# Optimization experiments

Measured on AMD Instinct MI355X. Metric: run time of the kernel, lower is better.

Reference implementation:

```python
import jax, jax.numpy as jnp
import numpy as np
from functools import partial

# Block hyperparams (match init_kwargs)
B, C, N, H = 16, 512, 1024, 8
HID = 4 * C
TAU, THRESH, SG_SCALE = 2.0, 1.0, 5.0
ATTN_SCALE = 0.25
BN_EPS = 1e-5

# LIF spiking neuron (single-step, stateless): membrane v = x / tau, hard threshold
# forward; sigmoid surrogate gradient (scale=5.0) in backward.
@partial(jax.custom_vjp, nondiff_argnums=(1,))
def spike(u, scale):
    return (u >= 0.0).astype(u.dtype)

def _spike_fwd(u, scale):
    return spike(u, scale), u

def _spike_bwd(scale, u, g):
    s = jax.nn.sigmoid(scale * u)
    return (g * scale * s * (1.0 - s),)

spike.defvjp(_spike_fwd, _spike_bwd)

def lif(x):
    return spike(x / TAU - THRESH, SG_SCALE)

def conv1x1(x, w, b=None):
    # x: [B,C,N], w: [O,C] -> [B,O,N]
    y = jnp.einsum('oc,bcn->bon', w, x)
    return y if b is None else y + b[None, :, None]

def bn(x, g, b):
    # BatchNorm1d, training-mode batch stats over (batch, length), biased var
    m = jnp.mean(x, axis=(0, 2), keepdims=True)
    v = jnp.var(x, axis=(0, 2), keepdims=True)
    return (x - m) * jax.lax.rsqrt(v + BN_EPS) * g[None, :, None] + b[None, :, None]


def setup_inputs() -> dict:
    key = jax.random.key(0)
    ks = jax.random.split(key, 8)
    w = lambda k, o, i: jax.random.normal(k, (o, i), dtype=jnp.float32) * 0.02
    inp = {
        'x': jax.random.normal(ks[0], (B, C, N), dtype=jnp.float32),
        'q_w': w(ks[1], C, C), 'q_g': jnp.ones((C,), jnp.float32), 'q_b': jnp.zeros((C,), jnp.float32),
        'k_w': w(ks[2], C, C), 'k_g': jnp.ones((C,), jnp.float32), 'k_b': jnp.zeros((C,), jnp.float32),
        'v_w': w(ks[3], C, C), 'v_g': jnp.ones((C,), jnp.float32), 'v_b': jnp.zeros((C,), jnp.float32),
        'proj_w': w(ks[4], C, C), 'proj_bias': jnp.zeros((C,), jnp.float32),
        'proj_g': jnp.ones((C,), jnp.float32), 'proj_b': jnp.zeros((C,), jnp.float32),
        'fc1_w': w(ks[5], HID, C), 'fc1_bias': jnp.zeros((HID,), jnp.float32),
        'fc1_g': jnp.ones((HID,), jnp.float32), 'fc1_b': jnp.zeros((HID,), jnp.float32),
        'fc2_w': w(ks[6], C, HID), 'fc2_bias': jnp.zeros((C,), jnp.float32),
        'fc2_g': jnp.ones((C,), jnp.float32), 'fc2_b': jnp.zeros((C,), jnp.float32),
    }
    return inp


def reference(x, q_w, q_g, q_b, k_w, k_g, k_b, v_w, v_g, v_b,
              proj_w, proj_bias, proj_g, proj_b,
              fc1_w, fc1_bias, fc1_g, fc1_b, fc2_w, fc2_bias, fc2_g, fc2_b):
    Bb, Cc, Nn = x.shape
    D = Cc // H

    def heads(t):  # [B,C,N] -> [B,H,N,D]
        return t.transpose(0, 2, 1).reshape(Bb, Nn, H, D).transpose(0, 2, 1, 3)

    # spiking attention (no softmax): (Q K^T) V * 0.25
    q = heads(lif(bn(conv1x1(x, q_w), q_g, q_b)))
    k = heads(lif(bn(conv1x1(x, k_w), k_g, k_b)))
    v = heads(lif(bn(conv1x1(x, v_w), v_g, v_b)))
    scores = jnp.einsum('bhnd,bhmd->bhnm', q, k)            # [B,H,N,N]
    attn = jnp.einsum('bhnm,bhmd->bhnd', scores, v) * ATTN_SCALE
    a = attn.transpose(0, 1, 3, 2).reshape(Bb, Cc, Nn)       # [B,C,N]
    a = lif(a)
    a = lif(bn(conv1x1(a, proj_w, proj_bias), proj_g, proj_b))
    x = x + a                                                # residual 1

    # conv1x1-BN-LIF MLP
    h = lif(bn(conv1x1(x, fc1_w, fc1_bias), fc1_g, fc1_b))
    h = lif(bn(conv1x1(h, fc2_w, fc2_bias), fc2_g, fc2_b))
    return x + h                                             # residual 2
```

## Files before the change

kernel.cpp:

```cpp
#include <hip/hip_runtime.h>
#include <stdint.h>

#pragma clang fp contract(off)

#define BATCH 16
#define CCH   512
#define NLEN  1024
#define NH    8
#define DH    64

__device__ float pw128(const float* __restrict__ x) {
    float r0=x[0],r1=x[1],r2=x[2],r3=x[3],r4=x[4],r5=x[5],r6=x[6],r7=x[7];
    for (int i = 8; i < 128; i += 8) {
        r0 += x[i+0]; r1 += x[i+1]; r2 += x[i+2]; r3 += x[i+3];
        r4 += x[i+4]; r5 += x[i+5]; r6 += x[i+6]; r7 += x[i+7];
    }
    return ((r0+r1)+(r2+r3))+((r4+r5)+(r6+r7));
}
__device__ float pw128_sqdev(const float* __restrict__ x, float m) {
    float r0,r1,r2,r3,r4,r5,r6,r7;
    {
        float d;
        d = x[0]-m; r0 = d*d;  d = x[1]-m; r1 = d*d;
        d = x[2]-m; r2 = d*d;  d = x[3]-m; r3 = d*d;
        d = x[4]-m; r4 = d*d;  d = x[5]-m; r5 = d*d;
        d = x[6]-m; r6 = d*d;  d = x[7]-m; r7 = d*d;
    }
    for (int i = 8; i < 128; i += 8) {
        float d;
        d = x[i+0]-m; r0 += d*d;  d = x[i+1]-m; r1 += d*d;
        d = x[i+2]-m; r2 += d*d;  d = x[i+3]-m; r3 += d*d;
        d = x[i+4]-m; r4 += d*d;  d = x[i+5]-m; r5 += d*d;
        d = x[i+6]-m; r6 += d*d;  d = x[i+7]-m; r7 += d*d;
    }
    return ((r0+r1)+(r2+r3))+((r4+r5)+(r6+r7));
}

__global__ __launch_bounds__(64) void bn_stats_np_k(const float* __restrict__ Y, int O,
                                                    float2* __restrict__ st)
{
    const int o = blockIdx.x;
    const int t = threadIdx.x;
    const int bi = t >> 2, q = t & 3;
    __shared__ float part[64];
    __shared__ float msh;
    const float* p = Y + ((size_t)bi * O + o) * NLEN + q * 256;
    {
        float s0 = pw128(p), s1 = pw128(p + 128);
        part[t] = s0 + s1;
    }
    __syncthreads();
    if (t == 0) {
        float s = 0.0f;
        for (int b = 0; b < 16; ++b) {
            const float* pp = &part[b * 4];
            float v = (pp[0] + pp[1]) + (pp[2] + pp[3]);
            s = (b == 0) ? v : (s + v);
        }
        msh = s / 16384.0f;
    }
    __syncthreads();
    const float m = msh;
    {
        float s0 = pw128_sqdev(p, m), s1 = pw128_sqdev(p + 128, m);
        part[t] = s0 + s1;
    }
    __syncthreads();
    if (t == 0) {
        float s = 0.0f;
        for (int b = 0; b < 16; ++b) {
            const float* pp = &part[b * 4];
            float v = (pp[0] + pp[1]) + (pp[2] + pp[3]);
            s = (b == 0) ? v : (s + v);
        }
        float var = s / 16384.0f;
        float ve  = var + 1e-5f;
        float sq  = (float)sqrt((double)ve);
        float r   = (float)(1.0 / (double)sq);
        st[o] = make_float2(m, r);
    }
}

__device__ inline bool spike_f32(float y, float2 s, float g, float b) {
    float t1 = y - s.x;
    float t2 = t1 * s.y;
    float t3 = t2 * g;
    float t4 = t3 + b;
    float u  = t4 / 2.0f - 1.0f;
    return u >= 0.0f;
}

template<int MODE>
__global__ __launch_bounds__(256) void gemm_k(
    const float* __restrict__ W, const float* __restrict__ Xf, const uint8_t* __restrict__ Xs8,
    const float* __restrict__ bias, float* __restrict__ Y,
    int O, int Cin, int N)
{
    __shared__ float Ws[32][132];
    __shared__ float Xs[32][132];
    const int b = blockIdx.z;
    const size_t xbase = (size_t)b * Cin * N;
    float* Yb = Y + (size_t)b * O * N;
    const int o0 = blockIdx.y * 128;
    const int n0 = blockIdx.x * 128;
    const int t  = threadIdx.x;
    const int tx = t & 15;
    const int ty = t >> 4;

    const int wr = t >> 1;
    const int wk = (t & 1) << 4;
    const int xk = t >> 3;
    const int xc = (t & 7) << 4;

    float acc[8][8];
#pragma unroll
    for (int i = 0; i < 8; ++i)
#pragma unroll
        for (int j = 0; j < 8; ++j) acc[i][j] = 0.0f;

    float4 wA[4];
    float  xr[16];

    auto loadG = [&](int k0) {
        const float* wp = W + (size_t)(o0 + wr) * Cin + k0 + wk;
#pragma unroll
        for (int j = 0; j < 4; ++j)
            wA[j] = *reinterpret_cast<const float4*>(wp + 4 * j);
        size_t off = xbase + (size_t)(k0 + xk) * N + n0 + xc;
#pragma unroll
        for (int j = 0; j < 4; ++j) {
            float4 v = *reinterpret_cast<const float4*>(Xf + off + 4 * j);
            if (MODE == 0) {
                xr[4*j+0]=v.x; xr[4*j+1]=v.y; xr[4*j+2]=v.z; xr[4*j+3]=v.w;
            } else {
                uchar4 u = *reinterpret_cast<const uchar4*>(Xs8 + off + 4 * j);
                xr[4*j+0]=v.x+(float)u.x; xr[4*j+1]=v.y+(float)u.y;
                xr[4*j+2]=v.z+(float)u.z; xr[4*j+3]=v.w+(float)u.w;
            }
        }
    };
    auto stage = [&]() {
#pragma unroll
        for (int j = 0; j < 4; ++j) {
            Ws[wk+4*j+0][wr] = wA[j].x;
            Ws[wk+4*j+1][wr] = wA[j].y;
            Ws[wk+4*j+2][wr] = wA[j].z;
            Ws[wk+4*j+3][wr] = wA[j].w;
        }
#pragma unroll
        for (int j = 0; j < 4; ++j)
            *reinterpret_cast<float4*>(&Xs[xk][xc + 4*j]) =
                make_float4(xr[4*j+0], xr[4*j+1], xr[4*j+2], xr[4*j+3]);
    };

    loadG(0);
    stage();
    __syncthreads();
    for (int k0 = 0;;) {
        const int kn = k0 + 32;
        const bool more = kn < Cin;
        if (more) loadG(kn);
#pragma unroll
        for (int kk = 0; kk < 32; ++kk) {
            float4 a0 = *reinterpret_cast<const float4*>(&Ws[kk][ty * 4]);
            float4 a1 = *reinterpret_cast<const float4*>(&Ws[kk][64 + ty * 4]);
            float4 b0 = *reinterpret_cast<const float4*>(&Xs[kk][tx * 4]);
            float4 b1 = *reinterpret_cast<const float4*>(&Xs[kk][64 + tx * 4]);
            float av[8] = {a0.x,a0.y,a0.z,a0.w,a1.x,a1.y,a1.z,a1.w};
            float bv[8] = {b0.x,b0.y,b0.z,b0.w,b1.x,b1.y,b1.z,b1.w};
#pragma unroll
            for (int i = 0; i < 8; ++i)
#pragma unroll
                for (int j = 0; j < 8; ++j)
                    acc[i][j] = fmaf(av[i], bv[j], acc[i][j]);
        }
        if (!more) break;
        __syncthreads();
        stage();
        __syncthreads();
        k0 = kn;
    }
#pragma unroll
    for (int half = 0; half < 2; ++half)
#pragma unroll
        for (int i = 0; i < 4; ++i) {
            const int r = half * 4 + i;
            const int o = o0 + half * 64 + ty * 4 + i;
            const float bb = bias ? bias[o] : 0.0f;
            float* yp = Yb + (size_t)o * N + n0;
            float4 r0, r1;
            r0.x = acc[r][0] + bb; r0.y = acc[r][1] + bb;
            r0.z = acc[r][2] + bb; r0.w = acc[r][3] + bb;
            r1.x = acc[r][4] + bb; r1.y = acc[r][5] + bb;
            r1.z = acc[r][6] + bb; r1.w = acc[r][7] + bb;
            *reinterpret_cast<float4*>(yp + tx * 4)      = r0;
            *reinterpret_cast<float4*>(yp + 64 + tx * 4) = r1;
        }
}

__global__ __launch_bounds__(256) void wt_k(const float* __restrict__ W, float* __restrict__ Wt,
                                            int O, int Cin)
{
    __shared__ float tile[32][33];
    const int k0 = blockIdx.x * 32, o0 = blockIdx.y * 32;
    const int tx = threadIdx.x & 31, ty = threadIdx.x >> 5;
#pragma unroll
    for (int j = 0; j < 4; ++j)
        tile[ty + 8*j][tx] = W[(size_t)(o0 + ty + 8*j) * Cin + k0 + tx];
    __syncthreads();
#pragma unroll
    for (int j = 0; j < 4; ++j)
        Wt[(size_t)(k0 + ty + 8*j) * O + o0 + tx] = tile[tx][ty + 8*j];
}

__global__ __launch_bounds__(256) void col_bits_k(const uint8_t* __restrict__ S,
                                                  unsigned long long* __restrict__ bits, int Cin)
{
    const int n0 = blockIdx.x * 64, kw = blockIdx.y, b = blockIdx.z;
    __shared__ uint8_t tile[64][64];
    const int t = threadIdx.x;
    const int r = t >> 2, cg = (t & 3) * 16;
    const uint8_t* src = S + ((size_t)b * Cin + kw * 64 + r) * NLEN + n0 + cg;
    *reinterpret_cast<uint4*>(&tile[r][cg]) = *reinterpret_cast<const uint4*>(src);
    __syncthreads();
    if (t < 64) {
        unsigned long long m = 0;
#pragma unroll
        for (int rr = 0; rr < 64; ++rr)
            m |= ((unsigned long long)(tile[rr][t] != 0)) << rr;
        bits[((size_t)b * NLEN + n0 + t) * (Cin >> 6) + kw] = m;
    }
}

__global__ __launch_bounds__(256) void sparse_gemm_k(
    const float* __restrict__ Wt, const unsigned long long* __restrict__ bits,
    const float* __restrict__ bias, float* __restrict__ Y, int Cin)
{
    const int wid  = (blockIdx.x << 2) + (threadIdx.x >> 6);
    const int lane = threadIdx.x & 63;
    const int b = wid >> 10, n = wid & 1023;
    const int W64 = Cin >> 6;
    float acc[8];
#pragma unroll
    for (int i = 0; i < 8; ++i) acc[i] = 0.0f;
    const unsigned long long* bp = bits + ((size_t)b * NLEN + n) * W64;
    for (int w = 0; w < W64; ++w) {
        unsigned long long m = bp[w];
        while (m) {
            const int bit = __builtin_ctzll(m);
            m &= m - 1;
            const int k = (w << 6) + bit;
            const float* wr = Wt + ((size_t)k << 9) + lane * 8;
            float4 w0 = *reinterpret_cast<const float4*>(wr);
            float4 w1 = *reinterpret_cast<const float4*>(wr + 4);
            acc[0] += w0.x; acc[1] += w0.y; acc[2] += w0.z; acc[3] += w0.w;
            acc[4] += w1.x; acc[5] += w1.y; acc[6] += w1.z; acc[7] += w1.w;
        }
    }
    const float* bq = bias + lane * 8;
    float4 b0 = *reinterpret_cast<const float4*>(bq);
    float4 b1 = *reinterpret_cast<const float4*>(bq + 4);
    float bi[8] = {b0.x, b0.y, b0.z, b0.w, b1.x, b1.y, b1.z, b1.w};
    float* yp = Y + ((size_t)b * 512 + lane * 8) * NLEN + n;
#pragma unroll
    for (int i = 0; i < 8; ++i)
        yp[(size_t)i * NLEN] = acc[i] + bi[i];
}

__global__ __launch_bounds__(256) void spike_pack_qkv_k(
    const float* __restrict__ Y, const float2* __restrict__ st,
    const float* __restrict__ gq, const float* __restrict__ gk, const float* __restrict__ gv,
    const float* __restrict__ bq, const float* __restrict__ bk, const float* __restrict__ bv,
    uint8_t* __restrict__ oq, uint8_t* __restrict__ ok, uint8_t* __restrict__ ov)
{
    const int nt = blockIdx.x, hs = blockIdx.y, b = blockIdx.z;
    const int tensor = hs >> 3, h = hs & 7;
    const float* g  = (tensor == 0) ? gq : (tensor == 1) ? gk : gv;
    const float* be = (tensor == 0) ? bq : (tensor == 1) ? bk : bv;
    uint8_t* outp   = (tensor == 0) ? oq : (tensor == 1) ? ok : ov;
    __shared__ uint8_t tile[64][68];
    const int t = threadIdx.x;
    {
        const int i = t & 63, dq = t >> 6;
#pragma unroll
        for (int p = 0; p < 16; ++p) {
            int d  = dq * 16 + p;
            int cf = hs * 64 + d;
            int cl = h * 64 + d;
            float y = Y[((size_t)b * 1536 + cf) * NLEN + nt * 64 + i];
            tile[d][i] = spike_f32(y, st[cf], g[cl], be[cl]) ? 1 : 0;
        }
    }
    __syncthreads();
    {
        const int d = t & 63, iq = t >> 6;
#pragma unroll
        for (int p = 0; p < 16; ++p) {
            int i = iq * 16 + p;
            outp[((size_t)(b * NH + h) * NLEN + nt * 64 + i) * DH + d] = tile[d][i];
        }
    }
}

__global__ __launch_bounds__(256) void ktv_k(const uint8_t* __restrict__ Kb, const uint8_t* __restrict__ Vb,
                                             float* __restrict__ M)
{
    const int bh = blockIdx.x;
    const uint8_t* kp = Kb + (size_t)bh * NLEN * DH;
    const uint8_t* vp = Vb + (size_t)bh * NLEN * DH;
    __shared__ float ks[64][68];
    __shared__ float vs[64][68];
    const int t = threadIdx.x;
    const int d2 = t & 63, g4 = t >> 6;
    float acc[16];
#pragma unroll
    for (int j = 0; j < 16; ++j) acc[j] = 0.f;

    for (int nc = 0; nc < NLEN; nc += 64) {
#pragma unroll
        for (int p = 0; p < 16; ++p) {
            int idx = t + p * 256;
            int r = idx >> 6, d = idx & 63;
            ks[r][d] = (float)kp[(size_t)(nc + r) * DH + d];
            vs[r][d] = (float)vp[(size_t)(nc + r) * DH + d];
        }
        __syncthreads();
        for (int n = 0; n < 64; ++n) {
            float vv = vs[n][d2];
#pragma unroll
            for (int j = 0; j < 16; ++j)
                acc[j] += ks[n][g4 * 16 + j] * vv;
        }
        __syncthreads();
    }
#pragma unroll
    for (int j = 0; j < 16; ++j)
        M[(size_t)bh * 4096 + (size_t)(g4 * 16 + j) * 64 + d2] = acc[j];
}

__global__ __launch_bounds__(256) void attn_spike_k(const uint8_t* __restrict__ Qb, const float* __restrict__ M,
                                                    uint8_t* __restrict__ A)
{
    const int nt = blockIdx.x, h = blockIdx.y, b = blockIdx.z;
    const int bh = b * NH + h;
    __shared__ float Ms[64][68];
    __shared__ float qs[64][65];
    const int t = threadIdx.x;
#pragma unroll
    for (int p = 0; p < 16; ++p) {
        int idx = t + p * 256;
        int r = idx >> 6, c = idx & 63;
        Ms[r][c] = M[(size_t)bh * 4096 + idx];
        qs[c][r] = (float)Qb[((size_t)bh * NLEN + nt * 64 + r) * DH + c];
    }
    __syncthreads();
    const int n = t & 63, dg = t >> 6;
    float acc[16];
#pragma unroll
    for (int j = 0; j < 16; ++j) acc[j] = 0.f;
    for (int d1 = 0; d1 < 64; ++d1) {
        float qv = qs[d1][n];
#pragma unroll
        for (int j = 0; j < 16; ++j)
            acc[j] += qv * Ms[d1][dg * 16 + j];
    }
#pragma unroll
    for (int j = 0; j < 16; ++j) {
        int d = dg * 16 + j;
        A[((size_t)b * CCH + h * 64 + d) * NLEN + nt * 64 + n] = (acc[j] >= 8.0f) ? 1 : 0;
    }
}

__global__ __launch_bounds__(256) void spike_store_k(
    const float* __restrict__ Y, const float2* __restrict__ st,
    const float* __restrict__ g, const float* __restrict__ bet,
    uint8_t* __restrict__ H, int Oc, int o_off, int Otot)
{
    size_t i4 = (size_t)blockIdx.x * 256 + threadIdx.x;
    size_t total = (size_t)BATCH * Oc * (NLEN / 4);
    if (i4 >= total) return;
    int n4 = (int)(i4 & 255);
    int o  = (int)((i4 >> 8) % Oc);
    int b  = (int)(i4 / ((size_t)256 * Oc));
    float4 y = reinterpret_cast<const float4*>(Y)[i4];
    float2 s = st[o];
    float gg = g[o], bb = bet[o];
    uchar4 r;
    r.x = spike_f32(y.x, s, gg, bb) ? 1 : 0;
    r.y = spike_f32(y.y, s, gg, bb) ? 1 : 0;
    r.z = spike_f32(y.z, s, gg, bb) ? 1 : 0;
    r.w = spike_f32(y.w, s, gg, bb) ? 1 : 0;
    *reinterpret_cast<uchar4*>(H + ((size_t)(b * Otot + o_off + o)) * NLEN + n4 * 4) = r;
}

__global__ __launch_bounds__(256) void final_k(
    const float* __restrict__ Y, const float2* __restrict__ st,
    const float* __restrict__ g, const float* __restrict__ bet,
    const float* __restrict__ x, const uint8_t* __restrict__ ares,
    float* __restrict__ Out)
{
    size_t i4 = (size_t)blockIdx.x * 256 + threadIdx.x;
    size_t total = (size_t)BATCH * CCH * (NLEN / 4);
    if (i4 >= total) return;
    int o = (int)((i4 >> 8) % CCH);
    float4 y  = reinterpret_cast<const float4*>(Y)[i4];
    float4 xv = reinterpret_cast<const float4*>(x)[i4];
    uchar4 av = reinterpret_cast<const uchar4*>(ares)[i4];
    float2 s = st[o];
    float gg = g[o], bb = bet[o];
    float4 r;
    {
        float x1;
        x1 = xv.x + (float)av.x; r.x = x1 + (spike_f32(y.x, s, gg, bb) ? 1.0f : 0.0f);
        x1 = xv.y + (float)av.y; r.y = x1 + (spike_f32(y.y, s, gg, bb) ? 1.0f : 0.0f);
        x1 = xv.z + (float)av.z; r.z = x1 + (spike_f32(y.z, s, gg, bb) ? 1.0f : 0.0f);
        x1 = xv.w + (float)av.w; r.w = x1 + (spike_f32(y.w, s, gg, bb) ? 1.0f : 0.0f);
    }
    reinterpret_cast<float4*>(Out)[i4] = r;
}

extern "C" void kernel_launch(void* const* d_in, const int* in_sizes, int n_in,
                              void* d_out, int out_size, void* d_ws, size_t ws_size,
                              hipStream_t stream)
{
    const float* x         = (const float*)d_in[0];
    const float* q_w       = (const float*)d_in[1];
    const float* q_g       = (const float*)d_in[2];
    const float* q_b       = (const float*)d_in[3];
    const float* k_w       = (const float*)d_in[4];
    const float* k_g       = (const float*)d_in[5];
    const float* k_b       = (const float*)d_in[6];
    const float* v_w       = (const float*)d_in[7];
    const float* v_g       = (const float*)d_in[8];
    const float* v_b       = (const float*)d_in[9];
    const float* proj_w    = (const float*)d_in[10];
    const float* proj_bias = (const float*)d_in[11];
    const float* proj_g    = (const float*)d_in[12];
    const float* proj_b    = (const float*)d_in[13];
    const float* fc1_w     = (const float*)d_in[14];
    const float* fc1_bias  = (const float*)d_in[15];
    const float* fc1_g     = (const float*)d_in[16];
    const float* fc1_b     = (const float*)d_in[17];
    const float* fc2_w     = (const float*)d_in[18];
    const float* fc2_bias  = (const float*)d_in[19];
    const float* fc2_g     = (const float*)d_in[20];
    const float* fc2_b     = (const float*)d_in[21];
    float* out = (float*)d_out;

    char* ws = (char*)d_ws;
    const size_t MiB = 1ull << 20;
    if (ws_size < 124 * MiB) return;

    float*    Yq    = (float*)(ws);
    float*    Af    = (float*)(ws);
    uint8_t*  ab    = (uint8_t*)(ws);
    uint8_t*  ares  = (uint8_t*)(ws + 64 * MiB);
    uint8_t*  hb    = (uint8_t*)(ws + 72 * MiB);
    uint8_t*  qb    = (uint8_t*)(ws + 96 * MiB);
    uint8_t*  kb    = (uint8_t*)(ws + 104 * MiB);
    uint8_t*  vb    = (uint8_t*)(ws + 112 * MiB);
    float*    Wt    = (float*)(ws + 104 * MiB);
    unsigned long long* bits = (unsigned long long*)(ws + 108 * MiB);
    float*    Wcat  = (float*)(ws + 120 * MiB);
    float*    Mbuf  = (float*)(ws + 120 * MiB);
    float2*   stats = (float2*)(ws + 123 * MiB);

    dim3 thr256(256);

    hipMemcpyAsync(Wcat,          q_w, (size_t)512 * 512 * 4, hipMemcpyDeviceToDevice, stream);
    hipMemcpyAsync(Wcat + 262144, k_w, (size_t)512 * 512 * 4, hipMemcpyDeviceToDevice, stream);
    hipMemcpyAsync(Wcat + 524288, v_w, (size_t)512 * 512 * 4, hipMemcpyDeviceToDevice, stream);
    gemm_k<0><<<dim3(8, 12, 16), thr256, 0, stream>>>(Wcat, x, nullptr, nullptr, Yq, 1536, 512, 1024);
    bn_stats_np_k<<<dim3(1536), dim3(64), 0, stream>>>(Yq, 1536, stats);
    spike_pack_qkv_k<<<dim3(16, 24, 16), thr256, 0, stream>>>(Yq, stats, q_g, k_g, v_g,
                                                              q_b, k_b, v_b, qb, kb, vb);

    ktv_k<<<dim3(128), thr256, 0, stream>>>(kb, vb, Mbuf);
    attn_spike_k<<<dim3(16, 8, 16), thr256, 0, stream>>>(qb, Mbuf, ab);

    wt_k<<<dim3(16, 16), thr256, 0, stream>>>(proj_w, Wt, 512, 512);
    col_bits_k<<<dim3(16, 8, 16), thr256, 0, stream>>>(ab, bits, 512);
    sparse_gemm_k<<<dim3(4096), thr256, 0, stream>>>(Wt, bits, proj_bias, Af, 512);
    bn_stats_np_k<<<dim3(512), dim3(64), 0, stream>>>(Af, 512, stats);
    spike_store_k<<<dim3(8192), thr256, 0, stream>>>(Af, stats, proj_g, proj_b, ares, 512, 0, 512);

    for (int ch = 0; ch < 2; ++ch) {
        gemm_k<2><<<dim3(8, 8, 16), thr256, 0, stream>>>(fc1_w + (size_t)ch * 1024 * 512, x, ares,
                                                         fc1_bias + ch * 1024, Af, 1024, 512, 1024);
        bn_stats_np_k<<<dim3(1024), dim3(64), 0, stream>>>(Af, 1024, stats);
        spike_store_k<<<dim3(16384), thr256, 0, stream>>>(Af, stats, fc1_g + ch * 1024, fc1_b + ch * 1024,
                                                          hb, 1024, ch * 1024, 2048);
    }

    wt_k<<<dim3(64, 16), thr256, 0, stream>>>(fc2_w, Wt, 512, 2048);
    col_bits_k<<<dim3(16, 32, 16), thr256, 0, stream>>>(hb, bits, 2048);
    sparse_gemm_k<<<dim3(4096), thr256, 0, stream>>>(Wt, bits, fc2_bias, Af, 2048);
    bn_stats_np_k<<<dim3(512), dim3(64), 0, stream>>>(Af, 512, stats);
    final_k<<<dim3(8192), thr256, 0, stream>>>(Af, stats, fc2_g, fc2_b, x, ares, out);
}
```

Measured before the change: 1.432 ms.

## Double-buffer GEMM shared tiles with K-step 16 and one barrier per step

Switches the fp32 GEMM kernel from a single 32-deep shared-memory tile to two 16-deep buffers. The next tile is staged into the alternate buffer right after compute, so each K step needs only one __syncthreads instead of two. Per-thread prefetch registers are halved. The trade-off is twice as many loop iterations and barriers over the same K range, with less unrolled work per step to hide global-load latency.

```diff
diff --git a/kernel.cpp b/kernel.cpp
--- a/kernel.cpp
+++ b/kernel.cpp
@@ -96,8 +96,8 @@
     const float* __restrict__ bias, float* __restrict__ Y,
     int O, int Cin, int N)
 {
-    __shared__ float Ws[32][132];
-    __shared__ float Xs[32][132];
+    __shared__ float Ws[2][16][132];
+    __shared__ float Xs[2][16][132];
     const int b = blockIdx.z;
     const size_t xbase = (size_t)b * Cin * N;
     float* Yb = Y + (size_t)b * O * N;
@@ -108,9 +108,9 @@
     const int ty = t >> 4;
 
     const int wr = t >> 1;
-    const int wk = (t & 1) << 4;
-    const int xk = t >> 3;
-    const int xc = (t & 7) << 4;
+    const int wk = (t & 1) << 3;
+    const int xk = t >> 4;
+    const int xc = (t & 15) << 3;
 
     float acc[8][8];
 #pragma unroll
@@ -118,54 +118,51 @@
 #pragma unroll
         for (int j = 0; j < 8; ++j) acc[i][j] = 0.0f;
 
-    float4 wA[4];
-    float  xr[16];
+    float4 wA[2];
+    float  xr[8];
 
     auto loadG = [&](int k0) {
         const float* wp = W + (size_t)(o0 + wr) * Cin + k0 + wk;
-#pragma unroll
-        for (int j = 0; j < 4; ++j)
-            wA[j] = *reinterpret_cast<const float4*>(wp + 4 * j);
+        wA[0] = *reinterpret_cast<const float4*>(wp);
+        wA[1] = *reinterpret_cast<const float4*>(wp + 4);
         size_t off = xbase + (size_t)(k0 + xk) * N + n0 + xc;
-#pragma unroll
-        for (int j = 0; j < 4; ++j) {
-            float4 v = *reinterpret_cast<const float4*>(Xf + off + 4 * j);
-            if (MODE == 0) {
-                xr[4*j+0]=v.x; xr[4*j+1]=v.y; xr[4*j+2]=v.z; xr[4*j+3]=v.w;
-            } else {
-                uchar4 u = *reinterpret_cast<const uchar4*>(Xs8 + off + 4 * j);
-                xr[4*j+0]=v.x+(float)u.x; xr[4*j+1]=v.y+(float)u.y;
-                xr[4*j+2]=v.z+(float)u.z; xr[4*j+3]=v.w+(float)u.w;
-            }
+        float4 v0 = *reinterpret_cast<const float4*>(Xf + off);
+        float4 v1 = *reinterpret_cast<const float4*>(Xf + off + 4);
+        if (MODE == 0) {
+            xr[0]=v0.x; xr[1]=v0.y; xr[2]=v0.z; xr[3]=v0.w;
+            xr[4]=v1.x; xr[5]=v1.y; xr[6]=v1.z; xr[7]=v1.w;
+        } else {
+            uchar4 u0 = *reinterpret_cast<const uchar4*>(Xs8 + off);
+            uchar4 u1 = *reinterpret_cast<const uchar4*>(Xs8 + off + 4);
+            xr[0]=v0.x+(float)u0.x; xr[1]=v0.y+(float)u0.y;
+            xr[2]=v0.z+(float)u0.z; xr[3]=v0.w+(float)u0.w;
+            xr[4]=v1.x+(float)u1.x; xr[5]=v1.y+(float)u1.y;
+            xr[6]=v1.z+(float)u1.z; xr[7]=v1.w+(float)u1.w;
         }
     };
-    auto stage = [&]() {
-#pragma unroll
-        for (int j = 0; j < 4; ++j) {
-            Ws[wk+4*j+0][wr] = wA[j].x;
-            Ws[wk+4*j+1][wr] = wA[j].y;
-            Ws[wk+4*j+2][wr] = wA[j].z;
-            Ws[wk+4*j+3][wr] = wA[j].w;
-        }
-#pragma unroll
-        for (int j = 0; j < 4; ++j)
-            *reinterpret_cast<float4*>(&Xs[xk][xc + 4*j]) =
-                make_float4(xr[4*j+0], xr[4*j+1], xr[4*j+2], xr[4*j+3]);
+    auto stage = [&](int buf) {
+        Ws[buf][wk+0][wr]=wA[0].x; Ws[buf][wk+1][wr]=wA[0].y;
+        Ws[buf][wk+2][wr]=wA[0].z; Ws[buf][wk+3][wr]=wA[0].w;
+        Ws[buf][wk+4][wr]=wA[1].x; Ws[buf][wk+5][wr]=wA[1].y;
+        Ws[buf][wk+6][wr]=wA[1].z; Ws[buf][wk+7][wr]=wA[1].w;
+        *reinterpret_cast<float4*>(&Xs[buf][xk][xc])     = make_float4(xr[0],xr[1],xr[2],xr[3]);
+        *reinterpret_cast<float4*>(&Xs[buf][xk][xc + 4]) = make_float4(xr[4],xr[5],xr[6],xr[7]);
     };
 
     loadG(0);
-    stage();
-    __syncthreads();
+    stage(0);
+    __syncthreads();
+    int cur = 0;
     for (int k0 = 0;;) {
-        const int kn = k0 + 32;
+        const int kn = k0 + 16;
         const bool more = kn < Cin;
         if (more) loadG(kn);
 #pragma unroll
-        for (int kk = 0; kk < 32; ++kk) {
-            float4 a0 = *reinterpret_cast<const float4*>(&Ws[kk][ty * 4]);
-            float4 a1 = *reinterpret_cast<const float4*>(&Ws[kk][64 + ty * 4]);
-            float4 b0 = *reinterpret_cast<const float4*>(&Xs[kk][tx * 4]);
-            float4 b1 = *reinterpret_cast<const float4*>(&Xs[kk][64 + tx * 4]);
+        for (int kk = 0; kk < 16; ++kk) {
+            float4 a0 = *reinterpret_cast<const float4*>(&Ws[cur][kk][ty * 4]);
+            float4 a1 = *reinterpret_cast<const float4*>(&Ws[cur][kk][64 + ty * 4]);
+            float4 b0 = *reinterpret_cast<const float4*>(&Xs[cur][kk][tx * 4]);
+            float4 b1 = *reinterpret_cast<const float4*>(&Xs[cur][kk][64 + tx * 4]);
             float av[8] = {a0.x,a0.y,a0.z,a0.w,a1.x,a1.y,a1.z,a1.w};
             float bv[8] = {b0.x,b0.y,b0.z,b0.w,b1.x,b1.y,b1.z,b1.w};
 #pragma unroll
@@ -175,9 +172,9 @@
                     acc[i][j] = fmaf(av[i], bv[j], acc[i][j]);
         }
         if (!more) break;
+        stage(cur ^ 1);
         __syncthreads();
-        stage();
-        __syncthreads();
+        cur ^= 1;
         k0 = kn;
     }
 #pragma unroll
```

Result: no change. 1.450 ms (+1.3%).
